# Performance work log

Hardware: AMD Instinct MI355X
Metric: run time of the kernel (lower is better)

Reference implementation:

```python
import jax, jax.numpy as jnp
import numpy as np

SPARSITY_RATIO = 0.3


def setup_inputs() -> dict:
    key = jax.random.key(0)
    adj = jax.random.normal(key, (8, 2048, 2048), dtype=jnp.float32)
    return {"adj": adj}


def reference(adj):
    # k largest entries kept per row along the last axis (training-mode path)
    N = adj.shape[-1]
    k = max(1, int(N * (1.0 - SPARSITY_RATIO)))
    flat = adj.reshape(-1, N)                      # [B*N, N]
    _, topk_idx = jax.lax.top_k(flat, k)            # [B*N, k]
    rows = jnp.arange(flat.shape[0])[:, None]       # [B*N, 1]
    mask = jnp.zeros_like(flat).at[rows, topk_idx].set(1.0)
    return adj * mask.reshape(adj.shape)
```

## Files before the change

### kernel.cpp

```cpp
#include <hip/hip_runtime.h>


static constexpr int ROW_N   = 2048;
static constexpr int K_KEEP  = 1433;
static constexpr int THREADS = 256;
static constexpr int EPT     = 8;

__device__ __forceinline__ unsigned ord_f32(unsigned b) {
    return (b & 0x80000000u) ? ~b : (b | 0x80000000u);
}
__device__ __forceinline__ unsigned unord_f32(unsigned o) {
    return (o & 0x80000000u) ? (o & 0x7fffffffu) : ~o;
}

__global__ __launch_bounds__(THREADS)
void topk_row_mask(const float* __restrict__ in, float* __restrict__ out) {
    const int row  = blockIdx.x;
    const int t    = threadIdx.x;
    const int lane = t & 63;
    const int w    = t >> 6;

    const float4* rin  = reinterpret_cast<const float4*>(in)  + (size_t)row * (ROW_N / 4);
    float4*       rout = reinterpret_cast<float4*>(out)       + (size_t)row * (ROW_N / 4);

    const float4 va = rin[t * 2 + 0];
    const float4 vb = rin[t * 2 + 1];

    unsigned u[EPT];
    u[0] = ord_f32(__float_as_uint(va.x));
    u[1] = ord_f32(__float_as_uint(va.y));
    u[2] = ord_f32(__float_as_uint(va.z));
    u[3] = ord_f32(__float_as_uint(va.w));
    u[4] = ord_f32(__float_as_uint(vb.x));
    u[5] = ord_f32(__float_as_uint(vb.y));
    u[6] = ord_f32(__float_as_uint(vb.z));
    u[7] = ord_f32(__float_as_uint(vb.w));

    __shared__ unsigned hist[256];
    __shared__ unsigned wtot[4];
    __shared__ unsigned bc_bin;
    __shared__ unsigned bc_krem;

    unsigned alive = 0xFFu;
    unsigned krem  = K_KEEP;
    unsigned tu    = 0;

    #pragma unroll
    for (int pass = 3; pass >= 0; --pass) {
        const int shift = pass * 8;

        hist[t] = 0;
        __syncthreads();

        #pragma unroll
        for (int i = 0; i < EPT; ++i) {
            if ((alive >> i) & 1u)
                atomicAdd(&hist[(u[i] >> shift) & 0xFFu], 1u);
        }
        __syncthreads();

        unsigned s = hist[t];
        #pragma unroll
        for (int d = 1; d < 64; d <<= 1) {
            unsigned o = __shfl_down(s, d);
            if (lane + d < 64) s += o;
        }
        if (lane == 0) wtot[w] = s;
        __syncthreads();
        unsigned later = 0;
        #pragma unroll
        for (int w2 = 0; w2 < 4; ++w2)
            if (w2 > w) later += wtot[w2];
        const unsigned S = s + later;

        unsigned Snext = __shfl_down(S, 1);
        if (lane == 63) Snext = later;
        if (t == 255)   Snext = 0;

        if (S >= krem && Snext < krem) {
            bc_bin  = (unsigned)t;
            bc_krem = krem - Snext;
        }
        __syncthreads();

        const unsigned b = bc_bin;
        krem = bc_krem;
        tu   = (tu << 8) | b;
        #pragma unroll
        for (int i = 0; i < EPT; ++i) {
            if (((u[i] >> shift) & 0xFFu) != b) alive &= ~(1u << i);
        }
    }

    unsigned cnt = 0;
    #pragma unroll
    for (int i = 0; i < EPT; ++i) cnt += (u[i] == tu) ? 1u : 0u;

    unsigned s2 = cnt;
    #pragma unroll
    for (int d = 1; d < 64; d <<= 1) {
        unsigned o = __shfl_up(s2, d);
        if (lane >= d) s2 += o;
    }
    if (lane == 63) wtot[w] = s2;
    __syncthreads();
    unsigned basew = 0;
    #pragma unroll
    for (int w2 = 0; w2 < 4; ++w2)
        if (w2 < w) basew += wtot[w2];
    unsigned rank = basew + s2 - cnt;

    float ov[EPT];
    #pragma unroll
    for (int i = 0; i < EPT; ++i) {
        bool keep;
        if (u[i] > tu) {
            keep = true;
        } else if (u[i] == tu) {
            keep = (rank < krem);
            rank++;
        } else {
            keep = false;
        }
        ov[i] = keep ? __uint_as_float(unord_f32(u[i])) : 0.0f;
    }

    rout[t * 2 + 0] = make_float4(ov[0], ov[1], ov[2], ov[3]);
    rout[t * 2 + 1] = make_float4(ov[4], ov[5], ov[6], ov[7]);
}

extern "C" void kernel_launch(void* const* d_in, const int* in_sizes, int n_in,
                              void* d_out, int out_size, void* d_ws, size_t ws_size,
                              hipStream_t stream) {
    const float* in  = (const float*)d_in[0];
    float*       out = (float*)d_out;
    const int rows = in_sizes[0] / ROW_N;
    hipLaunchKernelGGL(topk_row_mask, dim3(rows), dim3(THREADS), 0, stream, in, out);
}
```

Before: 247.6 us.

## Switch radix select to 11/11/10-bit passes with early exit on unique pivot

Replaces the four 8-bit radix-select passes with two 11-bit passes and an optional 10-bit pass, using 2048-bin shared histograms scanned with 8 bins per thread. When the second pass leaves exactly one candidate, the third pass is skipped and the pivot is broadcast directly. When all pivot-equal elements are kept, the tie-ranking prefix scan is skipped. The output uses the original float values instead of un-mapping the keys. This cuts barrier rounds and passes, at the cost of larger histograms and more per-thread scan work.

```diff
diff --git a/kernel.cpp b/kernel.cpp
--- a/kernel.cpp
+++ b/kernel.cpp
@@ -6,15 +6,93 @@
 static constexpr int THREADS = 256;
 static constexpr int EPT     = 8;
 
+struct Smem {
+    alignas(16) unsigned hist[2048];
+    unsigned wtot[4];
+    unsigned bc_bin, bc_krem, bc_cnt;
+};
+
 __device__ __forceinline__ unsigned ord_f32(unsigned b) {
-    return (b & 0x80000000u) ? ~b : (b | 0x80000000u);
+    unsigned m = (unsigned)((int)b >> 31);
+    return b ^ (m | 0x80000000u);
 }
-__device__ __forceinline__ unsigned unord_f32(unsigned o) {
-    return (o & 0x80000000u) ? (o & 0x7fffffffu) : ~o;
+
+template<int SHIFT, int NBITS, bool LAST>
+__device__ __forceinline__ void radix_pass(Smem* sm, const unsigned (&u)[EPT],
+                                           unsigned& alive, unsigned& krem,
+                                           unsigned& tu, unsigned& cnt,
+                                           int t, int lane, int w)
+{
+    constexpr int BINS = 1 << NBITS;
+    constexpr int BPT  = BINS / THREADS;
+    constexpr unsigned DMASK = (unsigned)(BINS - 1);
+
+    uint4* hv = reinterpret_cast<uint4*>(&sm->hist[t * BPT]);
+    #pragma unroll
+    for (int i = 0; i < BPT / 4; ++i) hv[i] = make_uint4(0u, 0u, 0u, 0u);
+    __syncthreads();
+
+    if (alive) {
+        #pragma unroll
+        for (int i = 0; i < EPT; ++i) {
+            if ((alive >> i) & 1u)
+                atomicAdd(&sm->hist[(u[i] >> SHIFT) & DMASK], 1u);
+        }
+    }
+    __syncthreads();
+
+    unsigned h[BPT];
+    #pragma unroll
+    for (int i = 0; i < BPT / 4; ++i) {
+        uint4 x = hv[i];
+        h[4*i+0] = x.x; h[4*i+1] = x.y; h[4*i+2] = x.z; h[4*i+3] = x.w;
+    }
+    unsigned T = 0;
+    #pragma unroll
+    for (int i = 0; i < BPT; ++i) T += h[i];
+
+    unsigned s = T;
+    #pragma unroll
+    for (int d = 1; d < 64; d <<= 1) {
+        unsigned o = __shfl_down(s, d);
+        s += (lane + d < 64) ? o : 0u;
+    }
+    if (lane == 0) sm->wtot[w] = s;
+    __syncthreads();
+
+    unsigned later = 0;
+    #pragma unroll
+    for (int w2 = 1; w2 < 4; ++w2)
+        later += (w2 > w) ? sm->wtot[w2] : 0u;
+
+    unsigned Snext = (s - T) + later;
+    #pragma unroll
+    for (int i = BPT - 1; i >= 0; --i) {
+        unsigned S = Snext + h[i];
+        if (S >= krem && Snext < krem) {
+            sm->bc_bin  = (unsigned)(t * BPT + i);
+            sm->bc_krem = krem - Snext;
+            sm->bc_cnt  = h[i];
+        }
+        Snext = S;
+    }
+    __syncthreads();
+
+    unsigned b = sm->bc_bin;
+    krem = sm->bc_krem;
+    cnt  = sm->bc_cnt;
+    tu  |= (b << SHIFT);
+    if (!LAST) {
+        #pragma unroll
+        for (int i = 0; i < EPT; ++i) {
+            if (((u[i] >> SHIFT) & DMASK) != b) alive &= ~(1u << i);
+        }
+    }
 }
 
 __global__ __launch_bounds__(THREADS)
 void topk_row_mask(const float* __restrict__ in, float* __restrict__ out) {
+    __shared__ Smem sm;
     const int row  = blockIdx.x;
     const int t    = threadIdx.x;
     const int lane = t & 63;
@@ -36,97 +114,79 @@
     u[6] = ord_f32(__float_as_uint(vb.z));
     u[7] = ord_f32(__float_as_uint(vb.w));
 
-    __shared__ unsigned hist[256];
-    __shared__ unsigned wtot[4];
-    __shared__ unsigned bc_bin;
-    __shared__ unsigned bc_krem;
-
     unsigned alive = 0xFFu;
     unsigned krem  = K_KEEP;
     unsigned tu    = 0;
+    unsigned cnt   = 0;
 
-    #pragma unroll
-    for (int pass = 3; pass >= 0; --pass) {
-        const int shift = pass * 8;
+    radix_pass<21, 11, false>(&sm, u, alive, krem, tu, cnt, t, lane, w);
+    radix_pass<10, 11, false>(&sm, u, alive, krem, tu, cnt, t, lane, w);
 
-        hist[t] = 0;
+    bool allkeep;
+    if (cnt == 1u) {
+        if (alive) {
+            #pragma unroll
+            for (int i = 0; i < EPT; ++i)
+                if ((alive >> i) & 1u) sm.wtot[0] = u[i];
+        }
         __syncthreads();
+        tu   = sm.wtot[0];
+        krem = 1u;
+        allkeep = true;
+    } else {
+        radix_pass<0, 10, true>(&sm, u, alive, krem, tu, cnt, t, lane, w);
+        allkeep = (krem == cnt);
+    }
 
+    if (allkeep) {
+        float4 oa, ob;
+        oa.x = (u[0] >= tu) ? va.x : 0.0f;
+        oa.y = (u[1] >= tu) ? va.y : 0.0f;
+        oa.z = (u[2] >= tu) ? va.z : 0.0f;
+        oa.w = (u[3] >= tu) ? va.w : 0.0f;
+        ob.x = (u[4] >= tu) ? vb.x : 0.0f;
+        ob.y = (u[5] >= tu) ? vb.y : 0.0f;
+        ob.z = (u[6] >= tu) ? vb.z : 0.0f;
+        ob.w = (u[7] >= tu) ? vb.w : 0.0f;
+        rout[t * 2 + 0] = oa;
+        rout[t * 2 + 1] = ob;
+    } else {
+        unsigned ce = 0;
+        #pragma unroll
+        for (int i = 0; i < EPT; ++i) ce += (u[i] == tu) ? 1u : 0u;
+
+        unsigned s2 = ce;
+        #pragma unroll
+        for (int d = 1; d < 64; d <<= 1) {
+            unsigned o = __shfl_up(s2, d);
+            s2 += (lane >= d) ? o : 0u;
+        }
+        if (lane == 63) sm.wtot[w] = s2;
+        __syncthreads();
+        unsigned basew = 0;
+        #pragma unroll
+        for (int w2 = 0; w2 < 3; ++w2)
+            basew += (w2 < w) ? sm.wtot[w2] : 0u;
+        unsigned rank = basew + s2 - ce;
+
+        const float orig[EPT] = {va.x, va.y, va.z, va.w, vb.x, vb.y, vb.z, vb.w};
+        float ov[EPT];
         #pragma unroll
         for (int i = 0; i < EPT; ++i) {
-            if ((alive >> i) & 1u)
-                atomicAdd(&hist[(u[i] >> shift) & 0xFFu], 1u);
+            bool keep;
+            if (u[i] > tu) {
+                keep = true;
+            } else if (u[i] == tu) {
+                keep = (rank < krem);
+                rank++;
+            } else {
+                keep = false;
+            }
+            ov[i] = keep ? orig[i] : 0.0f;
         }
-        __syncthreads();
-
-        unsigned s = hist[t];
-        #pragma unroll
-        for (int d = 1; d < 64; d <<= 1) {
-            unsigned o = __shfl_down(s, d);
-            if (lane + d < 64) s += o;
-        }
-        if (lane == 0) wtot[w] = s;
-        __syncthreads();
-        unsigned later = 0;
-        #pragma unroll
-        for (int w2 = 0; w2 < 4; ++w2)
-            if (w2 > w) later += wtot[w2];
-        const unsigned S = s + later;
-
-        unsigned Snext = __shfl_down(S, 1);
-        if (lane == 63) Snext = later;
-        if (t == 255)   Snext = 0;
-
-        if (S >= krem && Snext < krem) {
-            bc_bin  = (unsigned)t;
-            bc_krem = krem - Snext;
-        }
-        __syncthreads();
-
-        const unsigned b = bc_bin;
-        krem = bc_krem;
-        tu   = (tu << 8) | b;
-        #pragma unroll
-        for (int i = 0; i < EPT; ++i) {
-            if (((u[i] >> shift) & 0xFFu) != b) alive &= ~(1u << i);
-        }
+        rout[t * 2 + 0] = make_float4(ov[0], ov[1], ov[2], ov[3]);
+        rout[t * 2 + 1] = make_float4(ov[4], ov[5], ov[6], ov[7]);
     }
-
-    unsigned cnt = 0;
-    #pragma unroll
-    for (int i = 0; i < EPT; ++i) cnt += (u[i] == tu) ? 1u : 0u;
-
-    unsigned s2 = cnt;
-    #pragma unroll
-    for (int d = 1; d < 64; d <<= 1) {
-        unsigned o = __shfl_up(s2, d);
-        if (lane >= d) s2 += o;
-    }
-    if (lane == 63) wtot[w] = s2;
-    __syncthreads();
-    unsigned basew = 0;
-    #pragma unroll
-    for (int w2 = 0; w2 < 4; ++w2)
-        if (w2 < w) basew += wtot[w2];
-    unsigned rank = basew + s2 - cnt;
-
-    float ov[EPT];
-    #pragma unroll
-    for (int i = 0; i < EPT; ++i) {
-        bool keep;
-        if (u[i] > tu) {
-            keep = true;
-        } else if (u[i] == tu) {
-            keep = (rank < krem);
-            rank++;
-        } else {
-            keep = false;
-        }
-        ov[i] = keep ? __uint_as_float(unord_f32(u[i])) : 0.0f;
-    }
-
-    rout[t * 2 + 0] = make_float4(ov[0], ov[1], ov[2], ov[3]);
-    rout[t * 2 + 1] = make_float4(ov[4], ov[5], ov[6], ov[7]);
 }
 
 extern "C" void kernel_launch(void* const* d_in, const int* in_sizes, int n_in,
```

Result: faster. 224.1 us (-9.5%).
